# Performance work log

Hardware: AMD Instinct MI355X
Metric: run time of the kernel (lower is better)

The kernel has to match this reference:

```python
import jax, jax.numpy as jnp
import numpy as np

N = 2_000_000
L = 8
K = 16
SIGMA = 0.1
POINT_ENCODING_SIZE = 20
FEAT = POINT_ENCODING_SIZE + (2 * L + 1) * 3 + (2 + 2 * K)  # 105


def setup_inputs() -> dict:
    key = jax.random.key(0)
    ks = jax.random.split(key, 9)
    bases = jax.random.uniform(ks[0], (N, 3), dtype=jnp.float32)
    normals = jax.random.uniform(ks[1], (N, 2), dtype=jnp.float32)
    encodings = jax.random.normal(ks[2], (N, POINT_ENCODING_SIZE), dtype=jnp.float32)
    # Linear params (Kaiming-uniform-ish scale)
    def lin(k, fan_in, fan_out):
        kw, kb = jax.random.split(k)
        bound = 1.0 / np.sqrt(fan_in)
        W = jax.random.uniform(kw, (fan_in, fan_out), minval=-bound, maxval=bound, dtype=jnp.float32)
        b = jax.random.uniform(kb, (fan_out,), minval=-bound, maxval=bound, dtype=jnp.float32)
        return W, b
    W1, b1 = lin(ks[3], FEAT, 64)
    W2, b2 = lin(ks[4], 64, 64)
    W3, b3 = lin(ks[5], 64, 3)
    return {"bases": bases, "normals": normals, "encodings": encodings,
            "W1": W1, "b1": b1, "W2": W2, "b2": b2, "W3": W3, "b3": b3}


def one_blob(s, T):
    # s: [N], T: [K] -> [N, K] Gaussian kernel
    d = s[:, None] - T[None, :]
    return jnp.exp(-(d * d) / (2.0 * SIGMA * SIGMA))


def reference(bases, normals, encodings, W1, b1, W2, b2, W3, b3):
    T = jnp.linspace(0.0, 1.0, K, dtype=jnp.float32)
    feats = [encodings, bases]
    for i in range(1, L + 1):
        f = (2.0 ** i) * bases
        feats += [jnp.sin(f), jnp.cos(f)]
    feats += [normals, one_blob(normals[:, 0], T), one_blob(normals[:, 1], T)]
    X = jnp.concatenate(feats, axis=-1)  # [N, 105]
    X = jnp.sin(X @ W1 + b1)
    X = jnp.sin(X @ W2 + b2)
    X = X @ W3 + b3
    return bases + X
```

## Files before the change

### kernel.cpp

```cpp
#include <hip/hip_runtime.h>
#include <hip/hip_bf16.h>
#include <stdint.h>


typedef unsigned short u16t;
typedef __attribute__((ext_vector_type(8))) short short8;
typedef __attribute__((ext_vector_type(4))) float f32x4;

#define GRID 3125
#define TPW  10

__device__ __forceinline__ float bf2f(u16t u) {
    union { uint32_t i; float f; } v; v.i = ((uint32_t)u) << 16; return v.f;
}
__device__ __forceinline__ u16t f2bf(float f) {
    __hip_bfloat16 h = __float2bfloat16(f);
    union { __hip_bfloat16 h; u16t u; } v; v.h = h; return v.u;
}

template<bool F32>
__device__ __forceinline__ float ldin(const void* p, int idx) {
    if (F32) return ((const float*)p)[idx];
    else     return bf2f(((const u16t*)p)[idx]);
}

template<bool F32>
__global__ __launch_bounds__(256, 2)
void nsub_mlp_kernel(const void* __restrict__ bases,
                     const void* __restrict__ normals,
                     const void* __restrict__ enc,
                     const void* __restrict__ W1, const void* __restrict__ b1,
                     const void* __restrict__ W2, const void* __restrict__ b2,
                     const void* __restrict__ W3, const void* __restrict__ b3,
                     void* __restrict__ out)
{
    {
        const uint32_t* pb = (const uint32_t*)bases;
        uint32_t m = 0;
        #pragma unroll
        for (int i = 0; i < 32; ++i) m |= pb[i];
        const bool is_f32 = (m & 0xC000u) != 0;
        if (is_f32 != F32) return;
    }

    __shared__ u16t Xs [4][16][136];
    __shared__ u16t Hs [4][16][72];
    __shared__ u16t H2s[4][16][72];

    const int tid  = threadIdx.x;
    const int wid  = tid >> 6;
    const int lane = tid & 63;
    const int q    = lane >> 4;
    const int col  = lane & 15;

    short8 w1f[4][4];
    #pragma unroll
    for (int kc = 0; kc < 4; ++kc)
      #pragma unroll
      for (int nt = 0; nt < 4; ++nt) {
        union { u16t u[8]; short8 v; } t;
        #pragma unroll
        for (int j = 0; j < 8; ++j) {
            const int k = kc*32 + q*8 + j;
            t.u[j] = (k < 105) ? f2bf(ldin<F32>(W1, k*64 + nt*16 + col)) : (u16t)0;
        }
        w1f[kc][nt] = t.v;
      }
    short8 w2f[2][4];
    #pragma unroll
    for (int kc = 0; kc < 2; ++kc)
      #pragma unroll
      for (int nt = 0; nt < 4; ++nt) {
        union { u16t u[8]; short8 v; } t;
        #pragma unroll
        for (int j = 0; j < 8; ++j) {
            const int k = kc*32 + q*8 + j;
            t.u[j] = f2bf(ldin<F32>(W2, k*64 + nt*16 + col));
        }
        w2f[kc][nt] = t.v;
      }
    short8 w3f[2];
    #pragma unroll
    for (int kc = 0; kc < 2; ++kc) {
        union { u16t u[8]; short8 v; } t;
        #pragma unroll
        for (int j = 0; j < 8; ++j) {
            const int k = kc*32 + q*8 + j;
            t.u[j] = (col < 3) ? f2bf(ldin<F32>(W3, k*3 + col)) : (u16t)0;
        }
        w3f[kc] = t.v;
    }
    float bias1[4], bias2[4];
    #pragma unroll
    for (int nt = 0; nt < 4; ++nt) {
        bias1[nt] = ldin<F32>(b1, nt*16 + col);
        bias2[nt] = ldin<F32>(b2, nt*16 + col);
    }
    const float bias3 = (col < 3) ? ldin<F32>(b3, col) : 0.0f;

    for (int t = 0; t < TPW; ++t) {
        const int tile = blockIdx.x*4 + wid + t*(GRID*4);
        const int row0 = tile << 4;

        {
            const int gr = row0 + col;
            u16t* xr = &Xs[wid][col][0];
            if (q == 0) {
                #pragma unroll
                for (int j = 0; j < 20; ++j) xr[j] = f2bf(ldin<F32>(enc, gr*20 + j));
                xr[20] = f2bf(ldin<F32>(bases, gr*3+0));
                xr[21] = f2bf(ldin<F32>(bases, gr*3+1));
                xr[22] = f2bf(ldin<F32>(bases, gr*3+2));
                xr[71] = f2bf(ldin<F32>(normals, gr*2+0));
                xr[72] = f2bf(ldin<F32>(normals, gr*2+1));
                #pragma unroll
                for (int j = 105; j < 136; ++j) xr[j] = 0;
            } else {
                const int c = q - 1;
                float f = ldin<F32>(bases, gr*3 + c);
                #pragma unroll
                for (int l = 0; l < 8; ++l) {
                    f *= 2.0f;
                    float s, co;
                    __sincosf(f, &s, &co);
                    xr[23 + l*6 + c]     = f2bf(s);
                    xr[23 + l*6 + 3 + c] = f2bf(co);
                }
                if (q == 1) {
                    const float n0 = ldin<F32>(normals, gr*2+0);
                    #pragma unroll
                    for (int k = 0; k < 16; ++k) {
                        const float d = n0 - (float)k*(1.0f/15.0f);
                        xr[73+k] = f2bf(__expf(-50.0f*d*d));
                    }
                } else if (q == 3) {
                    const float n1 = ldin<F32>(normals, gr*2+1);
                    #pragma unroll
                    for (int k = 0; k < 16; ++k) {
                        const float d = n1 - (float)k*(1.0f/15.0f);
                        xr[89+k] = f2bf(__expf(-50.0f*d*d));
                    }
                }
            }
        }
        __syncthreads();

        {
            f32x4 acc[4];
            #pragma unroll
            for (int nt = 0; nt < 4; ++nt)
                acc[nt] = (f32x4){bias1[nt], bias1[nt], bias1[nt], bias1[nt]};
            #pragma unroll
            for (int kc = 0; kc < 4; ++kc) {
                const short8 a = *(const short8*)(&Xs[wid][col][kc*32 + q*8]);
                #pragma unroll
                for (int nt = 0; nt < 4; ++nt)
                    acc[nt] = __builtin_amdgcn_mfma_f32_16x16x32_bf16(a, w1f[kc][nt], acc[nt], 0, 0, 0);
            }
            #pragma unroll
            for (int nt = 0; nt < 4; ++nt)
              #pragma unroll
              for (int i = 0; i < 4; ++i)
                  Hs[wid][q*4 + i][nt*16 + col] = f2bf(__sinf(acc[nt][i]));
        }
        __syncthreads();

        {
            f32x4 acc[4];
            #pragma unroll
            for (int nt = 0; nt < 4; ++nt)
                acc[nt] = (f32x4){bias2[nt], bias2[nt], bias2[nt], bias2[nt]};
            #pragma unroll
            for (int kc = 0; kc < 2; ++kc) {
                const short8 a = *(const short8*)(&Hs[wid][col][kc*32 + q*8]);
                #pragma unroll
                for (int nt = 0; nt < 4; ++nt)
                    acc[nt] = __builtin_amdgcn_mfma_f32_16x16x32_bf16(a, w2f[kc][nt], acc[nt], 0, 0, 0);
            }
            #pragma unroll
            for (int nt = 0; nt < 4; ++nt)
              #pragma unroll
              for (int i = 0; i < 4; ++i)
                  H2s[wid][q*4 + i][nt*16 + col] = f2bf(__sinf(acc[nt][i]));
        }
        __syncthreads();

        {
            f32x4 acc = (f32x4){bias3, bias3, bias3, bias3};
            #pragma unroll
            for (int kc = 0; kc < 2; ++kc) {
                const short8 a = *(const short8*)(&H2s[wid][col][kc*32 + q*8]);
                acc = __builtin_amdgcn_mfma_f32_16x16x32_bf16(a, w3f[kc], acc, 0, 0, 0);
            }
            if (col < 3) {
                #pragma unroll
                for (int i = 0; i < 4; ++i) {
                    const int r2 = row0 + q*4 + i;
                    const float res = ldin<F32>(bases, r2*3 + col) + acc[i];
                    if (F32) ((float*)out)[r2*3 + col] = res;
                    else     ((u16t*)out)[r2*3 + col] = f2bf(res);
                }
            }
        }
    }
}

extern "C" void kernel_launch(void* const* d_in, const int* in_sizes, int n_in,
                              void* d_out, int out_size, void* d_ws, size_t ws_size,
                              hipStream_t stream) {
    const void* bases   = d_in[0];
    const void* normals = d_in[1];
    const void* enc     = d_in[2];
    const void* W1      = d_in[3];
    const void* b1      = d_in[4];
    const void* W2      = d_in[5];
    const void* b2      = d_in[6];
    const void* W3      = d_in[7];
    const void* b3      = d_in[8];
    nsub_mlp_kernel<true ><<<GRID, 256, 0, stream>>>(bases, normals, enc, W1, b1, W2, b2, W3, b3, d_out);
    nsub_mlp_kernel<false><<<GRID, 256, 0, stream>>>(bases, normals, enc, W1, b1, W2, b2, W3, b3, d_out);
}
```

Baseline: 536.2 us.

## Use single-wave blocks, drop dtype-detection dual launch, specialize to fp32

Blocks shrink from four waves to one 64-thread wave, and the grid grows to match, so each __syncthreads is effectively a single-wave barrier. This removes stalls where waves wait on each other. The runtime dtype sniffing and the second template launch are removed, which saves a kernel launch and the probe loads. The kernel now assumes fp32 inputs, and each block still loads the full weight fragments into registers, so the weight-loading overhead per block is now spread over one wave instead of four.

Result: slower. 800.6 us (+49.3%).

```diff
diff --git a/kernel.cpp b/kernel.cpp
--- a/kernel.cpp
+++ b/kernel.cpp
@@ -7,49 +7,31 @@
 typedef __attribute__((ext_vector_type(8))) short short8;
 typedef __attribute__((ext_vector_type(4))) float f32x4;
 
-#define GRID 3125
+#define GRID 12500
 #define TPW  10
 
-__device__ __forceinline__ float bf2f(u16t u) {
-    union { uint32_t i; float f; } v; v.i = ((uint32_t)u) << 16; return v.f;
-}
 __device__ __forceinline__ u16t f2bf(float f) {
     __hip_bfloat16 h = __float2bfloat16(f);
     union { __hip_bfloat16 h; u16t u; } v; v.h = h; return v.u;
 }
-
-template<bool F32>
-__device__ __forceinline__ float ldin(const void* p, int idx) {
-    if (F32) return ((const float*)p)[idx];
-    else     return bf2f(((const u16t*)p)[idx]);
+__device__ __forceinline__ float bf2f(u16t u) {
+    union { uint32_t i; float f; } v; v.i = ((uint32_t)u) << 16; return v.f;
 }
 
-template<bool F32>
-__global__ __launch_bounds__(256, 2)
-void nsub_mlp_kernel(const void* __restrict__ bases,
-                     const void* __restrict__ normals,
-                     const void* __restrict__ enc,
-                     const void* __restrict__ W1, const void* __restrict__ b1,
-                     const void* __restrict__ W2, const void* __restrict__ b2,
-                     const void* __restrict__ W3, const void* __restrict__ b3,
-                     void* __restrict__ out)
+__global__ __launch_bounds__(64, 4)
+void nsub_mlp_kernel(const float* __restrict__ bases,
+                     const float* __restrict__ normals,
+                     const float* __restrict__ enc,
+                     const float* __restrict__ W1, const float* __restrict__ b1,
+                     const float* __restrict__ W2, const float* __restrict__ b2,
+                     const float* __restrict__ W3, const float* __restrict__ b3,
+                     float* __restrict__ out)
 {
-    {
-        const uint32_t* pb = (const uint32_t*)bases;
-        uint32_t m = 0;
-        #pragma unroll
-        for (int i = 0; i < 32; ++i) m |= pb[i];
-        const bool is_f32 = (m & 0xC000u) != 0;
-        if (is_f32 != F32) return;
-    }
+    __shared__ u16t Xs [16][136];
+    __shared__ u16t Hs [16][72];
+    __shared__ u16t H2s[16][72];
 
-    __shared__ u16t Xs [4][16][136];
-    __shared__ u16t Hs [4][16][72];
-    __shared__ u16t H2s[4][16][72];
-
-    const int tid  = threadIdx.x;
-    const int wid  = tid >> 6;
-    const int lane = tid & 63;
+    const int lane = threadIdx.x;
     const int q    = lane >> 4;
     const int col  = lane & 15;
 
@@ -62,7 +44,7 @@
         #pragma unroll
         for (int j = 0; j < 8; ++j) {
             const int k = kc*32 + q*8 + j;
-            t.u[j] = (k < 105) ? f2bf(ldin<F32>(W1, k*64 + nt*16 + col)) : (u16t)0;
+            t.u[j] = (k < 105) ? f2bf(W1[k*64 + nt*16 + col]) : (u16t)0;
         }
         w1f[kc][nt] = t.v;
       }
@@ -75,7 +57,7 @@
         #pragma unroll
         for (int j = 0; j < 8; ++j) {
             const int k = kc*32 + q*8 + j;
-            t.u[j] = f2bf(ldin<F32>(W2, k*64 + nt*16 + col));
+            t.u[j] = f2bf(W2[k*64 + nt*16 + col]);
         }
         w2f[kc][nt] = t.v;
       }
@@ -86,38 +68,38 @@
         #pragma unroll
         for (int j = 0; j < 8; ++j) {
             const int k = kc*32 + q*8 + j;
-            t.u[j] = (col < 3) ? f2bf(ldin<F32>(W3, k*3 + col)) : (u16t)0;
+            t.u[j] = (col < 3) ? f2bf(W3[k*3 + col]) : (u16t)0;
         }
         w3f[kc] = t.v;
     }
     float bias1[4], bias2[4];
     #pragma unroll
     for (int nt = 0; nt < 4; ++nt) {
-        bias1[nt] = ldin<F32>(b1, nt*16 + col);
-        bias2[nt] = ldin<F32>(b2, nt*16 + col);
+        bias1[nt] = b1[nt*16 + col];
+        bias2[nt] = b2[nt*16 + col];
     }
-    const float bias3 = (col < 3) ? ldin<F32>(b3, col) : 0.0f;
+    const float bias3 = (col < 3) ? b3[col] : 0.0f;
 
     for (int t = 0; t < TPW; ++t) {
-        const int tile = blockIdx.x*4 + wid + t*(GRID*4);
+        const int tile = blockIdx.x + t*GRID;
         const int row0 = tile << 4;
 
         {
             const int gr = row0 + col;
-            u16t* xr = &Xs[wid][col][0];
+            u16t* xr = &Xs[col][0];
             if (q == 0) {
                 #pragma unroll
-                for (int j = 0; j < 20; ++j) xr[j] = f2bf(ldin<F32>(enc, gr*20 + j));
-                xr[20] = f2bf(ldin<F32>(bases, gr*3+0));
-                xr[21] = f2bf(ldin<F32>(bases, gr*3+1));
-                xr[22] = f2bf(ldin<F32>(bases, gr*3+2));
-                xr[71] = f2bf(ldin<F32>(normals, gr*2+0));
-                xr[72] = f2bf(ldin<F32>(normals, gr*2+1));
+                for (int j = 0; j < 20; ++j) xr[j] = f2bf(enc[gr*20 + j]);
+                xr[20] = f2bf(bases[gr*3+0]);
+                xr[21] = f2bf(bases[gr*3+1]);
+                xr[22] = f2bf(bases[gr*3+2]);
+                xr[71] = f2bf(normals[gr*2+0]);
+                xr[72] = f2bf(normals[gr*2+1]);
                 #pragma unroll
                 for (int j = 105; j < 136; ++j) xr[j] = 0;
             } else {
                 const int c = q - 1;
-                float f = ldin<F32>(bases, gr*3 + c);
+                float f = bases[gr*3 + c];
                 #pragma unroll
                 for (int l = 0; l < 8; ++l) {
                     f *= 2.0f;
@@ -127,14 +109,14 @@
                     xr[23 + l*6 + 3 + c] = f2bf(co);
                 }
                 if (q == 1) {
-                    const float n0 = ldin<F32>(normals, gr*2+0);
+                    const float n0 = normals[gr*2+0];
                     #pragma unroll
                     for (int k = 0; k < 16; ++k) {
                         const float d = n0 - (float)k*(1.0f/15.0f);
                         xr[73+k] = f2bf(__expf(-50.0f*d*d));
                     }
                 } else if (q == 3) {
-                    const float n1 = ldin<F32>(normals, gr*2+1);
+                    const float n1 = normals[gr*2+1];
                     #pragma unroll
                     for (int k = 0; k < 16; ++k) {
                         const float d = n1 - (float)k*(1.0f/15.0f);
@@ -152,7 +134,7 @@
                 acc[nt] = (f32x4){bias1[nt], bias1[nt], bias1[nt], bias1[nt]};
             #pragma unroll
             for (int kc = 0; kc < 4; ++kc) {
-                const short8 a = *(const short8*)(&Xs[wid][col][kc*32 + q*8]);
+                const short8 a = *(const short8*)(&Xs[col][kc*32 + q*8]);
                 #pragma unroll
                 for (int nt = 0; nt < 4; ++nt)
                     acc[nt] = __builtin_amdgcn_mfma_f32_16x16x32_bf16(a, w1f[kc][nt], acc[nt], 0, 0, 0);
@@ -161,7 +143,7 @@
             for (int nt = 0; nt < 4; ++nt)
               #pragma unroll
               for (int i = 0; i < 4; ++i)
-                  Hs[wid][q*4 + i][nt*16 + col] = f2bf(__sinf(acc[nt][i]));
+                  Hs[q*4 + i][nt*16 + col] = f2bf(__sinf(acc[nt][i]));
         }
         __syncthreads();
 
@@ -172,7 +154,7 @@
                 acc[nt] = (f32x4){bias2[nt], bias2[nt], bias2[nt], bias2[nt]};
             #pragma unroll
             for (int kc = 0; kc < 2; ++kc) {
-                const short8 a = *(const short8*)(&Hs[wid][col][kc*32 + q*8]);
+                const short8 a = *(const short8*)(&Hs[col][kc*32 + q*8]);
                 #pragma unroll
                 for (int nt = 0; nt < 4; ++nt)
                     acc[nt] = __builtin_amdgcn_mfma_f32_16x16x32_bf16(a, w2f[kc][nt], acc[nt], 0, 0, 0);
@@ -181,7 +163,7 @@
             for (int nt = 0; nt < 4; ++nt)
               #pragma unroll
               for (int i = 0; i < 4; ++i)
-                  H2s[wid][q*4 + i][nt*16 + col] = f2bf(__sinf(acc[nt][i]));
+                  H2s[q*4 + i][nt*16 + col] = f2bf(__sinf(acc[nt][i]));
         }
         __syncthreads();
 
@@ -189,16 +171,15 @@
             f32x4 acc = (f32x4){bias3, bias3, bias3, bias3};
             #pragma unroll
             for (int kc = 0; kc < 2; ++kc) {
-                const short8 a = *(const short8*)(&H2s[wid][col][kc*32 + q*8]);
+                const short8 a = *(const short8*)(&H2s[col][kc*32 + q*8]);
                 acc = __builtin_amdgcn_mfma_f32_16x16x32_bf16(a, w3f[kc], acc, 0, 0, 0);
             }
             if (col < 3) {
                 #pragma unroll
                 for (int i = 0; i < 4; ++i) {
                     const int r2 = row0 + q*4 + i;
-                    const float res = ldin<F32>(bases, r2*3 + col) + acc[i];
-                    if (F32) ((float*)out)[r2*3 + col] = res;
-                    else     ((u16t*)out)[r2*3 + col] = f2bf(res);
+                    const float res = bases[r2*3 + col] + acc[i];
+                    out[r2*3 + col] = res;
                 }
             }
         }
@@ -208,15 +189,10 @@
 extern "C" void kernel_launch(void* const* d_in, const int* in_sizes, int n_in,
                               void* d_out, int out_size, void* d_ws, size_t ws_size,
                               hipStream_t stream) {
-    const void* bases   = d_in[0];
-    const void* normals = d_in[1];
-    const void* enc     = d_in[2];
-    const void* W1      = d_in[3];
-    const void* b1      = d_in[4];
-    const void* W2      = d_in[5];
-    const void* b2      = d_in[6];
-    const void* W3      = d_in[7];
-    const void* b3      = d_in[8];
-    nsub_mlp_kernel<true ><<<GRID, 256, 0, stream>>>(bases, normals, enc, W1, b1, W2, b2, W3, b3, d_out);
-    nsub_mlp_kernel<false><<<GRID, 256, 0, stream>>>(bases, normals, enc, W1, b1, W2, b2, W3, b3, d_out);
+    nsub_mlp_kernel<<<GRID, 64, 0, stream>>>(
+        (const float*)d_in[0], (const float*)d_in[1], (const float*)d_in[2],
+        (const float*)d_in[3], (const float*)d_in[4],
+        (const float*)d_in[5], (const float*)d_in[6],
+        (const float*)d_in[7], (const float*)d_in[8],
+        (float*)d_out);
 }
```
